# Kernel tuning notes

Measured on AMD Instinct MI355X. Metric: run time of the kernel, lower is better.

The kernel has to match this reference:

```python
import jax, jax.numpy as jnp
import numpy as np

NUM_HEADS = 8
D_HEAD = 64
ATTENTION_WINDOW = 512


def alibi_bias(num_heads, q_len, k_len):
    # ALiBi slopes for power-of-2 number of heads (Press et al. 2021).
    start = 2.0 ** (-(2.0 ** -(np.log2(num_heads) - 3.0)))
    slopes = jnp.asarray([start * (start ** i) for i in range(num_heads)],
                         dtype=jnp.float32)  # [H]
    rel = jnp.arange(q_len)[:, None] - jnp.arange(k_len)[None, :]  # [t, T]
    # Bidirectional ALiBi: bias = -slope * |i - j|
    return -slopes[:, None, None] * jnp.abs(rel).astype(jnp.float32)  # [H, t, T]


def sliding_window_mask(seq_len, window):
    # Attend to tokens within window//2 on each side; even window -> window+1.
    if window % 2 == 0:
        window += 1
    half = window // 2
    idx = jnp.arange(seq_len)
    return jnp.abs(idx[:, None] - idx[None, :]) <= half  # [S, S] bool


def setup_inputs() -> dict:
    key = jax.random.key(0)
    ks = jax.random.split(key, 6)
    B, S, E = 2, 4096, 512
    HD = NUM_HEADS * D_HEAD
    s_in = 1.0 / np.sqrt(E)
    s_out = 1.0 / np.sqrt(HD)
    return {
        'inputs_q': jax.random.normal(ks[0], (B, S, E), jnp.float32),
        'inputs_kv': jax.random.normal(ks[1], (B, S, E), jnp.float32),
        'w_q': jax.random.normal(ks[2], (E, HD), jnp.float32) * s_in,
        'w_k': jax.random.normal(ks[3], (E, HD), jnp.float32) * s_in,
        'w_v': jax.random.normal(ks[4], (E, HD), jnp.float32) * s_in,
        'w_o': jax.random.normal(ks[5], (HD, E), jnp.float32) * s_out,
    }


def reference(inputs_q, inputs_kv, w_q, w_k, w_v, w_o):
    B, S, E = inputs_q.shape
    H, D = NUM_HEADS, D_HEAD
    q = (inputs_q @ w_q).reshape(B, S, H, D)
    k = (inputs_kv @ w_k).reshape(B, S, H, D)
    v = (inputs_kv @ w_v).reshape(B, S, H, D)
    # scores: [B, H, t, T]
    att = jnp.einsum('bthd,bThd->bhtT', q, k) * (1.0 / jnp.sqrt(jnp.float32(D)))
    att = att + alibi_bias(H, S, S)[None]
    mask = sliding_window_mask(S, ATTENTION_WINDOW)
    att = jnp.where(mask[None, None], att, jnp.finfo(jnp.float32).min)
    p = jax.nn.softmax(att, axis=-1)
    out = jnp.einsum('bhtT,bThd->bthd', p, v).reshape(B, S, H * D)
    return out @ w_o
```

## Files before the change

### kernel.cpp

```cpp
#include <hip/hip_runtime.h>

#define S_LEN  4096
#define NH     8
#define DH     64
#define EMB    512
#define HDIM   512
#define HALF_W 256
#define BATCH  2
#define M_ROWS (BATCH * S_LEN)

typedef __attribute__((ext_vector_type(8))) short bf16x8;
typedef __attribute__((ext_vector_type(4))) float f32x4;

#define LOG2E 1.44269504088896f

__device__ __forceinline__ float b2f(unsigned short u) {
    union { unsigned int i; float f; } v; v.i = ((unsigned int)u) << 16; return v.f;
}
__device__ __forceinline__ unsigned short f2b(float f) {
    unsigned int x = __float_as_uint(f);
    unsigned int r = (x + 0x7fffu + ((x >> 16) & 1u)) >> 16;
    return (unsigned short)r;
}
__device__ __forceinline__ unsigned int f2bpk(float a, float b) {
    return ((__float_as_uint(a) + 0x8000u) >> 16) |
           ((__float_as_uint(b) + 0x8000u) & 0xffff0000u);
}
__device__ __forceinline__ void unpack2(unsigned int u, float* d) {
    d[0] = b2f((unsigned short)(u & 0xffffu));
    d[1] = b2f((unsigned short)(u >> 16));
}
union FragU { uint4 u; bf16x8 f; };
__device__ __forceinline__ bf16x8 ldfrag(const unsigned short* p) {
    FragU x; x.u = *(const uint4*)p; return x.f;
}

__device__ __forceinline__ void async16(const unsigned short* g, unsigned short* l) {
    __builtin_amdgcn_global_load_lds(
        (__attribute__((address_space(1))) void*)const_cast<unsigned short*>(g),
        (__attribute__((address_space(3))) void*)l, 16, 0, 0);
}

__device__ __forceinline__ int detect_flag(const unsigned short* __restrict__ xq) {
    __shared__ int s_flag;
    if (threadIdx.x == 0) s_flag = 0;
    __syncthreads();
    uint4 u = *(const uint4*)(xq + threadIdx.x * 8);
    const unsigned short* us = (const unsigned short*)&u;
    int bad = 0;
#pragma unroll
    for (int i = 0; i < 8; ++i) {
        float v = b2f(us[i]);
        if (!(fabsf(v) < 1.0e6f)) bad = 1;
    }
    if (__any(bad) && (threadIdx.x & 63) == 0) atomicOr(&s_flag, 1);
    __syncthreads();
    return s_flag;
}

__global__ __launch_bounds__(256) void prep(
    const void* __restrict__ xq, const void* __restrict__ xkv,
    const void* __restrict__ w0, const void* __restrict__ w1,
    const void* __restrict__ w2, const void* __restrict__ w3,
    unsigned short* __restrict__ Wt, unsigned short* __restrict__ Xc)
{
    const int flag = detect_flag((const unsigned short*)xq);
    const int blk = blockIdx.x;
    if (blk < 1024) {
        __shared__ float t[32][33];
        const int z = blk >> 8, idx = blk & 255;
        const void* src = (z == 0) ? w0 : (z == 1) ? w1 : (z == 2) ? w2 : w3;
        unsigned short* dst = Wt + (size_t)z * EMB * EMB;
        const int n0 = (idx & 15) << 5, k0 = (idx >> 4) << 5;
        const int kk = threadIdx.x >> 3;
        const int n4 = (threadIdx.x & 7) << 2;
        if (flag) {
            float4 v = *(const float4*)((const float*)src + (size_t)(k0 + kk) * EMB + n0 + n4);
            t[kk][n4] = v.x; t[kk][n4 + 1] = v.y; t[kk][n4 + 2] = v.z; t[kk][n4 + 3] = v.w;
        } else {
            uint2 u = *(const uint2*)((const unsigned short*)src + (size_t)(k0 + kk) * EMB + n0 + n4);
            unpack2(u.x, &t[kk][n4]); unpack2(u.y, &t[kk][n4 + 2]);
        }
        __syncthreads();
        const int nn = threadIdx.x >> 3;
        const int ks = (threadIdx.x & 7) << 2;
        uint2 pk;
        pk.x = (unsigned int)f2b(t[ks + 0][nn]) | ((unsigned int)f2b(t[ks + 1][nn]) << 16);
        pk.y = (unsigned int)f2b(t[ks + 2][nn]) | ((unsigned int)f2b(t[ks + 3][nn]) << 16);
        *(uint2*)(dst + (size_t)(n0 + nn) * EMB + k0 + ks) = pk;
    } else {
        if (!flag) return;
        const int idx = blk - 1024;
        const int z = idx >> 11;
        const float* src = (const float*)(z ? xkv : xq);
        unsigned short* dst = Xc + (size_t)z * M_ROWS * EMB;
        const size_t base = ((size_t)(idx & 2047) * 256 + threadIdx.x) * 8;
        float4 a = *(const float4*)(src + base);
        float4 b = *(const float4*)(src + base + 4);
        uint4 pk;
        pk.x = (unsigned int)f2b(a.x) | ((unsigned int)f2b(a.y) << 16);
        pk.y = (unsigned int)f2b(a.z) | ((unsigned int)f2b(a.w) << 16);
        pk.z = (unsigned int)f2b(b.x) | ((unsigned int)f2b(b.y) << 16);
        pk.w = (unsigned int)f2b(b.z) | ((unsigned int)f2b(b.w) << 16);
        *(uint4*)(dst + base) = pk;
    }
}

__device__ __forceinline__ void mgemm_core3(
    const unsigned short* __restrict__ A, const unsigned short* __restrict__ Bt,
    int m0, f32x4 (*acc)[4],
    unsigned short (*A_lds)[32], unsigned short (*B_lds)[32])
{
    const int tid  = threadIdx.x;
    const int lane = tid & 63;
    const int w    = tid >> 6;
    const int wm   = (w >> 1) << 6;
    const int wn   = (w & 1) << 6;
    const int qcol = lane & 15;
    const int quad = lane >> 4;

    const int arow = (w << 4) + (lane >> 2);
    const int acol = (lane & 3) << 3;

    const unsigned short* gA = A  + (size_t)(m0 + arow) * EMB + acol;
    const unsigned short* gB = Bt + (size_t)arow * EMB + acol;
    unsigned short* lA0 = &A_lds[arow][acol];
    unsigned short* lA1 = &A_lds[64 + arow][acol];
    unsigned short* lB0 = &B_lds[arow][acol];
    unsigned short* lB1 = &B_lds[64 + arow][acol];
    const size_t half = (size_t)64 * EMB;

    for (int k0 = 0; k0 < EMB; k0 += 32) {
        __syncthreads();
        async16(gA + k0, lA0);
        async16(gA + half + k0, lA1);
        async16(gB + k0, lB0);
        async16(gB + half + k0, lB1);
        __syncthreads();

        bf16x8 af[4], bf[4];
#pragma unroll
        for (int i = 0; i < 4; ++i) af[i] = ldfrag(&A_lds[wm + (i << 4) + qcol][quad * 8]);
#pragma unroll
        for (int j = 0; j < 4; ++j) bf[j] = ldfrag(&B_lds[wn + (j << 4) + qcol][quad * 8]);
#pragma unroll
        for (int i = 0; i < 4; ++i)
#pragma unroll
            for (int j = 0; j < 4; ++j)
                acc[i][j] = __builtin_amdgcn_mfma_f32_16x16x32_bf16(af[i], bf[j], acc[i][j], 0, 0, 0);
    }
}

__global__ __launch_bounds__(256) void gemm_qkv(
    const void* __restrict__ xq, const void* __restrict__ xkv,
    const unsigned short* __restrict__ Xc, const unsigned short* __restrict__ Wt,
    unsigned short* __restrict__ Qb, unsigned short* __restrict__ Kb,
    unsigned short* __restrict__ Vtb)
{
    const int flag = detect_flag((const unsigned short*)xq);
    __shared__ __align__(16) unsigned short A_lds[128][32];
    __shared__ __align__(16) unsigned short B_lds[128][32];
    const int blk = blockIdx.x;
    const int xcd = blk & 7, idx = blk >> 3;
    const int mi = idx / 12, ni = idx - mi * 12;
    const int m0 = ((xcd << 3) + mi) << 7;
    const int n0 = ni << 7;

    const unsigned short* A;
    if (flag) A = Xc + (n0 < 512 ? (size_t)0 : (size_t)M_ROWS * EMB);
    else      A = (const unsigned short*)(n0 < 512 ? xq : xkv);
    const unsigned short* Bt = Wt + (size_t)n0 * EMB;

    f32x4 acc[4][4];
#pragma unroll
    for (int i = 0; i < 4; ++i)
#pragma unroll
        for (int j = 0; j < 4; ++j) acc[i][j] = (f32x4){0.f, 0.f, 0.f, 0.f};

    mgemm_core3(A, Bt, m0, acc, A_lds, B_lds);

    const int lane = threadIdx.x & 63, w = threadIdx.x >> 6;
    const int wm = (w >> 1) << 6, wn = (w & 1) << 6;
    const int qcol = lane & 15, quad = lane >> 4;
    const int mode = (n0 < 512) ? 0 : (n0 < 1024) ? 1 : 2;
    const float qscale = 0.125f * LOG2E;
#pragma unroll
    for (int ms = 0; ms < 4; ++ms)
#pragma unroll
        for (int ns = 0; ns < 4; ++ns)
#pragma unroll
            for (int r = 0; r < 4; ++r) {
                const int m = m0 + wm + (ms << 4) + (quad << 2) + r;
                const int n = n0 + wn + (ns << 4) + qcol;
                if (mode == 0) {
                    Qb[(size_t)m * HDIM + n] = f2b(acc[ms][ns][r] * qscale);
                } else if (mode == 1) {
                    Kb[(size_t)m * HDIM + (n - 512)] = f2b(acc[ms][ns][r]);
                } else {
                    const int hd = n - 1024;
                    const int bb = m >> 12, s = m & (S_LEN - 1);
                    const int hh = hd >> 6, d = hd & 63;
                    Vtb[((size_t)((bb * NH + hh) * DH + d)) * S_LEN + s] = f2b(acc[ms][ns][r]);
                }
            }
}

__global__ __launch_bounds__(256) void gemm_out(
    const void* __restrict__ xq,
    const unsigned short* __restrict__ A, const unsigned short* __restrict__ Bt,
    void* __restrict__ C)
{
    const int flag = detect_flag((const unsigned short*)xq);
    __shared__ __align__(16) unsigned short A_lds[128][32];
    __shared__ __align__(16) unsigned short B_lds[128][32];
    const int blk = blockIdx.x;
    const int xcd = blk & 7, idx = blk >> 3;
    const int mi = idx >> 2, ni = idx & 3;
    const int m0 = ((xcd << 3) + mi) << 7;
    const int n0 = ni << 7;

    f32x4 acc[4][4];
#pragma unroll
    for (int i = 0; i < 4; ++i)
#pragma unroll
        for (int j = 0; j < 4; ++j) acc[i][j] = (f32x4){0.f, 0.f, 0.f, 0.f};

    mgemm_core3(A, Bt + (size_t)n0 * EMB, m0, acc, A_lds, B_lds);

    const int lane = threadIdx.x & 63, w = threadIdx.x >> 6;
    const int wm = (w >> 1) << 6, wn = (w & 1) << 6;
    const int qcol = lane & 15, quad = lane >> 4;
#pragma unroll
    for (int ms = 0; ms < 4; ++ms)
#pragma unroll
        for (int ns = 0; ns < 4; ++ns)
#pragma unroll
            for (int r = 0; r < 4; ++r) {
                const int m = m0 + wm + (ms << 4) + (quad << 2) + r;
                const int n = n0 + wn + (ns << 4) + qcol;
                const float v = acc[ms][ns][r];
                if (flag) ((float*)C)[(size_t)m * HDIM + n] = v;
                else      ((unsigned short*)C)[(size_t)m * HDIM + n] = f2b(v);
            }
}

__device__ __forceinline__ void attn_issue(
    const unsigned short* __restrict__ Kg, const unsigned short* __restrict__ Vt,
    int b, int h, int j0,
    unsigned short (*Kb)[64], unsigned short (*Vb)[64], int srow, int sp)
{
#pragma unroll
    for (int i = 0; i < 2; ++i) {
        const int row  = (i << 5) + srow;
        const int gseg = (sp ^ (row & 7)) << 3;
        const int jc = min(max(j0 + row, 0), S_LEN - 1);
        async16(Kg + (size_t)(b * S_LEN + jc) * HDIM + h * DH + gseg, &Kb[row][sp << 3]);
        const int js = min(max(j0 + gseg, 0), S_LEN - 8);
        async16(Vt + ((size_t)((b * NH + h) * DH + row)) * S_LEN + js, &Vb[row][sp << 3]);
    }
}

__global__ __launch_bounds__(256) void attn_mfma(
    const unsigned short* __restrict__ Q,
    const unsigned short* __restrict__ Kg,
    const unsigned short* __restrict__ Vt,
    unsigned short* __restrict__ O)
{
    __shared__ __align__(16) unsigned short K_lds[2][64][64];
    __shared__ __align__(16) unsigned short V_lds[2][64][64];
    __shared__ __align__(16) unsigned short P_lds[4][32][72];

    const int tid  = threadIdx.x;
    const int lane = tid & 63;
    const int w    = tid >> 6;
    const int blk  = blockIdx.x;
    const int bh   = blk >> 5;
    const int r5   = blk & 31;
    const int tile = ((r5 & 7) << 2) | (r5 >> 3);
    const int h    = bh & (NH - 1);
    const int b    = bh >> 3;
    const int t0   = tile << 7;
    const int tq0  = t0 + (w << 5);

    const int qcol = lane & 15;
    const int quad = lane >> 4;
    const float slope2 = LOG2E / (float)(2 << h);
    const float bias2  = 12.0f * LOG2E;

    bf16x8 qf[2][2];
#pragma unroll
    for (int qs = 0; qs < 2; ++qs) {
        const unsigned short* qrow =
            Q + (size_t)(b * S_LEN + tq0 + (qs << 4) + qcol) * HDIM + h * DH;
        qf[qs][0] = ldfrag(qrow + quad * 8);
        qf[qs][1] = ldfrag(qrow + 32 + quad * 8);
    }

    f32x4 Oacc[2][4];
#pragma unroll
    for (int qs = 0; qs < 2; ++qs)
#pragma unroll
        for (int i = 0; i < 4; ++i) Oacc[qs][i] = (f32x4){0.f, 0.f, 0.f, 0.f};
    float lsum[2] = {0.f, 0.f};

    const int srow = tid >> 3;
    const int sp   = tid & 7;

    attn_issue(Kg, Vt, b, h, t0 - HALF_W, K_lds[0], V_lds[0], srow, sp);

    for (int c = 0; c < 10; ++c) {
        const int j0 = t0 - HALF_W + (c << 6);
        __syncthreads();
        if (c < 9)
            attn_issue(Kg, Vt, b, h, j0 + 64,
                       K_lds[(c + 1) & 1], V_lds[(c + 1) & 1], srow, sp);
        const int bi = c & 1;

        if (j0 + 63 < tq0 - HALF_W || j0 > tq0 + 31 + HALF_W) continue;

#pragma unroll
        for (int qs = 0; qs < 2; ++qs) {
            const int qv = tq0 + (qs << 4) + qcol;
#pragma unroll
            for (int ks = 0; ks < 4; ++ks) {
                const int sj0 = j0 + (ks << 4);
                unsigned short* pdst = &P_lds[w][(qs << 4) + qcol][(ks << 4) + (quad << 2)];
                if (sj0 + 15 < tq0 + (qs << 4) - HALF_W ||
                    sj0 > tq0 + (qs << 4) + 15 + HALF_W) {
                    *(uint2*)pdst = (uint2){0u, 0u};
                    continue;
                }
                const int krow = (ks << 4) + qcol;
                const bf16x8 kf0 = ldfrag(&K_lds[bi][krow][(quad ^ (krow & 7)) << 3]);
                const bf16x8 kf1 = ldfrag(&K_lds[bi][krow][((4 + quad) ^ (krow & 7)) << 3]);
                f32x4 z = (f32x4){0.f, 0.f, 0.f, 0.f};
                z = __builtin_amdgcn_mfma_f32_16x16x32_bf16(kf0, qf[qs][0], z, 0, 0, 0);
                z = __builtin_amdgcn_mfma_f32_16x16x32_bf16(kf1, qf[qs][1], z, 0, 0, 0);
                float p[4];
#pragma unroll
                for (int r = 0; r < 4; ++r) {
                    const int j  = sj0 + (quad << 2) + r;
                    const int dd = qv - j;
                    const int ad = dd < 0 ? -dd : dd;
                    const bool ok = (ad <= HALF_W) && ((unsigned)j < (unsigned)S_LEN);
                    const float arg = fmaf(-slope2, (float)ad, z[r] - bias2);
                    const float e = exp2f(arg);
                    p[r] = ok ? e : 0.0f;
                    lsum[qs] += p[r];
                }
                uint2 pk;
                pk.x = f2bpk(p[0], p[1]);
                pk.y = f2bpk(p[2], p[3]);
                *(uint2*)pdst = pk;
            }
        }
#pragma unroll
        for (int qs = 0; qs < 2; ++qs) {
            const bf16x8 pf0 = ldfrag(&P_lds[w][(qs << 4) + qcol][quad * 8]);
            const bf16x8 pf1 = ldfrag(&P_lds[w][(qs << 4) + qcol][32 + quad * 8]);
#pragma unroll
            for (int ds = 0; ds < 4; ++ds) {
                const int vrow = (ds << 4) + qcol;
                const bf16x8 vf0 = ldfrag(&V_lds[bi][vrow][(quad ^ (vrow & 7)) << 3]);
                const bf16x8 vf1 = ldfrag(&V_lds[bi][vrow][((4 + quad) ^ (vrow & 7)) << 3]);
                Oacc[qs][ds] = __builtin_amdgcn_mfma_f32_16x16x32_bf16(vf0, pf0, Oacc[qs][ds], 0, 0, 0);
                Oacc[qs][ds] = __builtin_amdgcn_mfma_f32_16x16x32_bf16(vf1, pf1, Oacc[qs][ds], 0, 0, 0);
            }
        }
    }

#pragma unroll
    for (int qs = 0; qs < 2; ++qs) {
        float l = lsum[qs];
        l += __shfl_xor(l, 16, 64);
        l += __shfl_xor(l, 32, 64);
        const float rz = 1.0f / l;
        unsigned short* obase =
            O + (size_t)(b * S_LEN + tq0 + (qs << 4) + qcol) * HDIM + h * DH;
#pragma unroll
        for (int ds = 0; ds < 4; ++ds) {
            uint2 pk;
            pk.x = f2bpk(Oacc[qs][ds][0] * rz, Oacc[qs][ds][1] * rz);
            pk.y = f2bpk(Oacc[qs][ds][2] * rz, Oacc[qs][ds][3] * rz);
            *(uint2*)(obase + (ds << 4) + (quad << 2)) = pk;
        }
    }
}

extern "C" void kernel_launch(void* const* d_in, const int* in_sizes, int n_in,
                              void* d_out, int out_size, void* d_ws, size_t ws_size,
                              hipStream_t stream) {
    const void* xq  = d_in[0];
    const void* xkv = d_in[1];
    const void* wq  = d_in[2];
    const void* wk  = d_in[3];
    const void* wv  = d_in[4];
    const void* wo  = d_in[5];

    unsigned short* Qb  = (unsigned short*)((char*)d_ws + 256);
    unsigned short* Kb  = Qb  + (size_t)M_ROWS * HDIM;
    unsigned short* Vtb = Kb  + (size_t)M_ROWS * HDIM;
    unsigned short* Wt  = Vtb + (size_t)M_ROWS * HDIM;
    unsigned short* Wto = Wt + (size_t)3 * EMB * EMB;
    unsigned short* Xc  = (unsigned short*)d_out;

    prep<<<1024 + 4096, 256, 0, stream>>>(xq, xkv, wq, wk, wv, wo, Wt, Xc);
    gemm_qkv<<<768, 256, 0, stream>>>(xq, xkv, Xc, Wt, Qb, Kb, Vtb);
    attn_mfma<<<BATCH * NH * (S_LEN / 128), 256, 0, stream>>>(Qb, Kb, Vtb, Qb);
    gemm_out<<<256, 256, 0, stream>>>(xq, Qb, Wto, d_out);
}
```

Measured before the change: 182.8 us.

## Fuse fp32-to-bf16 input conversion into QKV GEMM and retile output GEMM

The QKV GEMM now reads fp32 activations directly, converts them to bf16 in registers and writes them to LDS. This removes the separate conversion pass in prep and the Xc round trip through memory. Separately, the output GEMM moves to 128x64 tiles with a 64-wide K step, XOR-swizzled LDS, and twice as many blocks for better occupancy across CUs. The cost is that A-operand loads in the QKV GEMM become synchronous register loads rather than async LDS copies, and each input is converted 12 times across the N tiles.

```diff
diff --git a/kernel.cpp b/kernel.cpp
--- a/kernel.cpp
+++ b/kernel.cpp
@@ -59,55 +59,39 @@
 }
 
 __global__ __launch_bounds__(256) void prep(
-    const void* __restrict__ xq, const void* __restrict__ xkv,
+    const void* __restrict__ xq,
     const void* __restrict__ w0, const void* __restrict__ w1,
     const void* __restrict__ w2, const void* __restrict__ w3,
-    unsigned short* __restrict__ Wt, unsigned short* __restrict__ Xc)
+    unsigned short* __restrict__ Wt)
 {
     const int flag = detect_flag((const unsigned short*)xq);
     const int blk = blockIdx.x;
-    if (blk < 1024) {
-        __shared__ float t[32][33];
-        const int z = blk >> 8, idx = blk & 255;
-        const void* src = (z == 0) ? w0 : (z == 1) ? w1 : (z == 2) ? w2 : w3;
-        unsigned short* dst = Wt + (size_t)z * EMB * EMB;
-        const int n0 = (idx & 15) << 5, k0 = (idx >> 4) << 5;
-        const int kk = threadIdx.x >> 3;
-        const int n4 = (threadIdx.x & 7) << 2;
-        if (flag) {
-            float4 v = *(const float4*)((const float*)src + (size_t)(k0 + kk) * EMB + n0 + n4);
-            t[kk][n4] = v.x; t[kk][n4 + 1] = v.y; t[kk][n4 + 2] = v.z; t[kk][n4 + 3] = v.w;
-        } else {
-            uint2 u = *(const uint2*)((const unsigned short*)src + (size_t)(k0 + kk) * EMB + n0 + n4);
-            unpack2(u.x, &t[kk][n4]); unpack2(u.y, &t[kk][n4 + 2]);
-        }
-        __syncthreads();
-        const int nn = threadIdx.x >> 3;
-        const int ks = (threadIdx.x & 7) << 2;
-        uint2 pk;
-        pk.x = (unsigned int)f2b(t[ks + 0][nn]) | ((unsigned int)f2b(t[ks + 1][nn]) << 16);
-        pk.y = (unsigned int)f2b(t[ks + 2][nn]) | ((unsigned int)f2b(t[ks + 3][nn]) << 16);
-        *(uint2*)(dst + (size_t)(n0 + nn) * EMB + k0 + ks) = pk;
+    __shared__ float t[32][33];
+    const int z = blk >> 8, idx = blk & 255;
+    const void* src = (z == 0) ? w0 : (z == 1) ? w1 : (z == 2) ? w2 : w3;
+    unsigned short* dst = Wt + (size_t)z * EMB * EMB;
+    const int n0 = (idx & 15) << 5, k0 = (idx >> 4) << 5;
+    const int kk = threadIdx.x >> 3;
+    const int n4 = (threadIdx.x & 7) << 2;
+    if (flag) {
+        float4 v = *(const float4*)((const float*)src + (size_t)(k0 + kk) * EMB + n0 + n4);
+        t[kk][n4] = v.x; t[kk][n4 + 1] = v.y; t[kk][n4 + 2] = v.z; t[kk][n4 + 3] = v.w;
     } else {
-        if (!flag) return;
-        const int idx = blk - 1024;
-        const int z = idx >> 11;
-        const float* src = (const float*)(z ? xkv : xq);
-        unsigned short* dst = Xc + (size_t)z * M_ROWS * EMB;
-        const size_t base = ((size_t)(idx & 2047) * 256 + threadIdx.x) * 8;
-        float4 a = *(const float4*)(src + base);
-        float4 b = *(const float4*)(src + base + 4);
-        uint4 pk;
-        pk.x = (unsigned int)f2b(a.x) | ((unsigned int)f2b(a.y) << 16);
-        pk.y = (unsigned int)f2b(a.z) | ((unsigned int)f2b(a.w) << 16);
-        pk.z = (unsigned int)f2b(b.x) | ((unsigned int)f2b(b.y) << 16);
-        pk.w = (unsigned int)f2b(b.z) | ((unsigned int)f2b(b.w) << 16);
-        *(uint4*)(dst + base) = pk;
-    }
-}
-
-__device__ __forceinline__ void mgemm_core3(
-    const unsigned short* __restrict__ A, const unsigned short* __restrict__ Bt,
+        uint2 u = *(const uint2*)((const unsigned short*)src + (size_t)(k0 + kk) * EMB + n0 + n4);
+        unpack2(u.x, &t[kk][n4]); unpack2(u.y, &t[kk][n4 + 2]);
+    }
+    __syncthreads();
+    const int nn = threadIdx.x >> 3;
+    const int ks = (threadIdx.x & 7) << 2;
+    uint2 pk;
+    pk.x = (unsigned int)f2b(t[ks + 0][nn]) | ((unsigned int)f2b(t[ks + 1][nn]) << 16);
+    pk.y = (unsigned int)f2b(t[ks + 2][nn]) | ((unsigned int)f2b(t[ks + 3][nn]) << 16);
+    *(uint2*)(dst + (size_t)(n0 + nn) * EMB + k0 + ks) = pk;
+}
+
+__device__ __forceinline__ void mgemm_core7(
+    const void* __restrict__ Av, int aFp32,
+    const unsigned short* __restrict__ Bt,
     int m0, f32x4 (*acc)[4],
     unsigned short (*A_lds)[32], unsigned short (*B_lds)[32])
 {
@@ -122,7 +106,6 @@
     const int arow = (w << 4) + (lane >> 2);
     const int acol = (lane & 3) << 3;
 
-    const unsigned short* gA = A  + (size_t)(m0 + arow) * EMB + acol;
     const unsigned short* gB = Bt + (size_t)arow * EMB + acol;
     unsigned short* lA0 = &A_lds[arow][acol];
     unsigned short* lA1 = &A_lds[64 + arow][acol];
@@ -130,12 +113,31 @@
     unsigned short* lB1 = &B_lds[64 + arow][acol];
     const size_t half = (size_t)64 * EMB;
 
+    const float* gAf = (const float*)Av + (size_t)(m0 + arow) * EMB + acol;
+    const unsigned short* gAb = (const unsigned short*)Av + (size_t)(m0 + arow) * EMB + acol;
+
     for (int k0 = 0; k0 < EMB; k0 += 32) {
         __syncthreads();
-        async16(gA + k0, lA0);
-        async16(gA + half + k0, lA1);
-        async16(gB + k0, lB0);
-        async16(gB + half + k0, lB1);
+        if (aFp32) {
+            float4 a0 = *(const float4*)(gAf + k0);
+            float4 a1 = *(const float4*)(gAf + k0 + 4);
+            float4 a2 = *(const float4*)(gAf + half + k0);
+            float4 a3 = *(const float4*)(gAf + half + k0 + 4);
+            async16(gB + k0, lB0);
+            async16(gB + half + k0, lB1);
+            uint4 u0, u1;
+            u0.x = f2bpk(a0.x, a0.y); u0.y = f2bpk(a0.z, a0.w);
+            u0.z = f2bpk(a1.x, a1.y); u0.w = f2bpk(a1.z, a1.w);
+            u1.x = f2bpk(a2.x, a2.y); u1.y = f2bpk(a2.z, a2.w);
+            u1.z = f2bpk(a3.x, a3.y); u1.w = f2bpk(a3.z, a3.w);
+            *(uint4*)lA0 = u0;
+            *(uint4*)lA1 = u1;
+        } else {
+            async16(gAb + k0, lA0);
+            async16(gAb + half + k0, lA1);
+            async16(gB + k0, lB0);
+            async16(gB + half + k0, lB1);
+        }
         __syncthreads();
 
         bf16x8 af[4], bf[4];
@@ -153,7 +155,7 @@
 
 __global__ __launch_bounds__(256) void gemm_qkv(
     const void* __restrict__ xq, const void* __restrict__ xkv,
-    const unsigned short* __restrict__ Xc, const unsigned short* __restrict__ Wt,
+    const unsigned short* __restrict__ Wt,
     unsigned short* __restrict__ Qb, unsigned short* __restrict__ Kb,
     unsigned short* __restrict__ Vtb)
 {
@@ -166,9 +168,7 @@
     const int m0 = ((xcd << 3) + mi) << 7;
     const int n0 = ni << 7;
 
-    const unsigned short* A;
-    if (flag) A = Xc + (n0 < 512 ? (size_t)0 : (size_t)M_ROWS * EMB);
-    else      A = (const unsigned short*)(n0 < 512 ? xq : xkv);
+    const void* A = (n0 < 512) ? xq : xkv;
     const unsigned short* Bt = Wt + (size_t)n0 * EMB;
 
     f32x4 acc[4][4];
@@ -177,7 +177,7 @@
 #pragma unroll
         for (int j = 0; j < 4; ++j) acc[i][j] = (f32x4){0.f, 0.f, 0.f, 0.f};
 
-    mgemm_core3(A, Bt, m0, acc, A_lds, B_lds);
+    mgemm_core7(A, flag, Bt, m0, acc, A_lds, B_lds);
 
     const int lane = threadIdx.x & 63, w = threadIdx.x >> 6;
     const int wm = (w >> 1) << 6, wn = (w & 1) << 6;
@@ -205,35 +205,90 @@
             }
 }
 
+__device__ __forceinline__ void mgemm_core4(
+    const unsigned short* __restrict__ A, const unsigned short* __restrict__ Bt,
+    int m0, f32x4 (*acc)[2],
+    unsigned short (*A_lds)[64], unsigned short (*B_lds)[64])
+{
+    const int tid  = threadIdx.x;
+    const int lane = tid & 63;
+    const int w    = tid >> 6;
+    const int wm   = (w >> 1) << 6;
+    const int wn   = (w & 1) << 5;
+    const int qcol = lane & 15;
+    const int quad = lane >> 4;
+    const int srow = tid >> 3;
+    const int sp   = tid & 7;
+
+    for (int k0 = 0; k0 < EMB; k0 += 64) {
+        __syncthreads();
+#pragma unroll
+        for (int i = 0; i < 4; ++i) {
+            const int row  = (i << 5) + srow;
+            const int gcol = ((sp ^ (row & 7)) << 3);
+            async16(A + (size_t)(m0 + row) * EMB + k0 + gcol, &A_lds[row][sp << 3]);
+        }
+#pragma unroll
+        for (int i = 0; i < 2; ++i) {
+            const int row  = (i << 5) + srow;
+            const int gcol = ((sp ^ (row & 7)) << 3);
+            async16(Bt + (size_t)row * EMB + k0 + gcol, &B_lds[row][sp << 3]);
+        }
+        __syncthreads();
+
+#pragma unroll
+        for (int kh = 0; kh < 2; ++kh) {
+            bf16x8 af[4], bf[2];
+#pragma unroll
+            for (int i = 0; i < 4; ++i) {
+                const int row = wm + (i << 4) + qcol;
+                const int p   = ((kh << 2) + quad) ^ (row & 7);
+                af[i] = ldfrag(&A_lds[row][p << 3]);
+            }
+#pragma unroll
+            for (int j = 0; j < 2; ++j) {
+                const int row = wn + (j << 4) + qcol;
+                const int p   = ((kh << 2) + quad) ^ (row & 7);
+                bf[j] = ldfrag(&B_lds[row][p << 3]);
+            }
+#pragma unroll
+            for (int i = 0; i < 4; ++i)
+#pragma unroll
+                for (int j = 0; j < 2; ++j)
+                    acc[i][j] = __builtin_amdgcn_mfma_f32_16x16x32_bf16(af[i], bf[j], acc[i][j], 0, 0, 0);
+        }
+    }
+}
+
 __global__ __launch_bounds__(256) void gemm_out(
     const void* __restrict__ xq,
     const unsigned short* __restrict__ A, const unsigned short* __restrict__ Bt,
     void* __restrict__ C)
 {
     const int flag = detect_flag((const unsigned short*)xq);
-    __shared__ __align__(16) unsigned short A_lds[128][32];
-    __shared__ __align__(16) unsigned short B_lds[128][32];
+    __shared__ __align__(16) unsigned short A_lds[128][64];
+    __shared__ __align__(16) unsigned short B_lds[64][64];
     const int blk = blockIdx.x;
     const int xcd = blk & 7, idx = blk >> 3;
-    const int mi = idx >> 2, ni = idx & 3;
+    const int mi = idx >> 3, ni = idx & 7;
     const int m0 = ((xcd << 3) + mi) << 7;
-    const int n0 = ni << 7;
-
-    f32x4 acc[4][4];
+    const int n0 = ni << 6;
+
+    f32x4 acc[4][2];
 #pragma unroll
     for (int i = 0; i < 4; ++i)
 #pragma unroll
-        for (int j = 0; j < 4; ++j) acc[i][j] = (f32x4){0.f, 0.f, 0.f, 0.f};
-
-    mgemm_core3(A, Bt + (size_t)n0 * EMB, m0, acc, A_lds, B_lds);
+        for (int j = 0; j < 2; ++j) acc[i][j] = (f32x4){0.f, 0.f, 0.f, 0.f};
+
+    mgemm_core4(A, Bt + (size_t)n0 * EMB, m0, acc, A_lds, B_lds);
 
     const int lane = threadIdx.x & 63, w = threadIdx.x >> 6;
-    const int wm = (w >> 1) << 6, wn = (w & 1) << 6;
+    const int wm = (w >> 1) << 6, wn = (w & 1) << 5;
     const int qcol = lane & 15, quad = lane >> 4;
 #pragma unroll
     for (int ms = 0; ms < 4; ++ms)
 #pragma unroll
-        for (int ns = 0; ns < 4; ++ns)
+        for (int ns = 0; ns < 2; ++ns)
 #pragma unroll
             for (int r = 0; r < 4; ++r) {
                 const int m = m0 + wm + (ms << 4) + (quad << 2) + r;
@@ -402,10 +457,9 @@
     unsigned short* Vtb = Kb  + (size_t)M_ROWS * HDIM;
     unsigned short* Wt  = Vtb + (size_t)M_ROWS * HDIM;
     unsigned short* Wto = Wt + (size_t)3 * EMB * EMB;
-    unsigned short* Xc  = (unsigned short*)d_out;
-
-    prep<<<1024 + 4096, 256, 0, stream>>>(xq, xkv, wq, wk, wv, wo, Wt, Xc);
-    gemm_qkv<<<768, 256, 0, stream>>>(xq, xkv, Xc, Wt, Qb, Kb, Vtb);
+
+    prep<<<1024, 256, 0, stream>>>(xq, wq, wk, wv, wo, Wt);
+    gemm_qkv<<<768, 256, 0, stream>>>(xq, xkv, Wt, Qb, Kb, Vtb);
     attn_mfma<<<BATCH * NH * (S_LEN / 128), 256, 0, stream>>>(Qb, Kb, Vtb, Qb);
-    gemm_out<<<256, 256, 0, stream>>>(xq, Qb, Wto, d_out);
-}
+    gemm_out<<<512, 256, 0, stream>>>(xq, Qb, Wto, d_out);
+}
```

Result: no change. 183.2 us (+0.2%).
